# Optimization experiments

Hardware: AMD Instinct MI355X
Metric: run time of the kernel (lower is better)

Reference implementation:

```python
import jax, jax.numpy as jnp
import numpy as np

C, H, N, B, L = 1, 512, 64, 16, 2048  # n_channels, n_heads, d_kernel, batch, seq_len


def setup_inputs() -> dict:
    key = jax.random.key(0)
    k1, k2 = jax.random.split(key)
    u = jax.random.normal(k1, (B, C * H, L), dtype=jnp.float32)
    k = jax.random.normal(k2, (C, H, N), dtype=jnp.float32)
    return {"u": u, "k": k}


def _l1_normalize(x, axis):
    # torch.linalg.norm(x, ord=1, dim=axis, keepdim=True): vector 1-norm along `axis`
    return x / jnp.sum(jnp.abs(x), axis=axis, keepdims=True)


def _forward(u, k):
    c, h, n = k.shape
    bsz, d, l = u.shape  # d == c*h
    dt = u.dtype
    # Shift matrix A: A[:, :, 1:, :-1] = I  (companion-style shift)
    A = jnp.zeros((c, h, n, n), dtype=dt).at[:, :, 1:, :-1].set(jnp.eye(n - 1, dtype=dt))
    # b = e1 broadcast to (c, h, n)
    b_vec = jnp.zeros((c, h, n), dtype=dt).at[:, :, 0].set(1.0)
    # closed-loop: k_norm = L1-normalize(clamp(k, 1/16, 1)); A_cl = L1-normalize(A + b k^T)
    k_norm = _l1_normalize(jnp.clip(k, 1.0 / 16.0, 1.0), axis=2)
    BK = jnp.einsum('chi,chj->chij', b_vec, k_norm)
    M = _l1_normalize(A + BK, axis=2)

    # Krylov recurrence: f[i] = k . (M^i b), i = 0..l-1
    def step(x, _):
        f_i = jnp.einsum('chn,chn->ch', k, x)
        x_next = jnp.einsum('chij,chj->chi', M, x)
        return x_next, f_i

    _, f = jax.lax.scan(step, b_vec, None, length=l)  # f: (l, c, h)
    f = jnp.moveaxis(f, 0, -1)  # (c, h, l)

    # Causal FFT convolution of u (b, c, h, l) with filter f (c, h, l)
    n_fft = 2 * l
    uf = jnp.fft.rfft(u.reshape(bsz, c, h, l), n=n_fft)
    ff = jnp.fft.rfft(f, n=n_fft)
    y = jnp.fft.irfft(uf * ff[None], n=n_fft)[..., :l]
    return y.reshape(bsz, c * h, l)


def reference(u, k):
    return _forward(u, k)
```

## Files before the change

### kernel.cpp

```cpp
#include <hip/hip_runtime.h>


namespace {

constexpr int kH = 512;
constexpr int kL = 2048;
constexpr int kChunks = 32;
constexpr int kStride = 68;

typedef __attribute__((ext_vector_type(8))) short bf16x8;
typedef __attribute__((ext_vector_type(4))) float f32x4;

__device__ inline unsigned short f32_to_bf16_rne(float x) {
  unsigned int u = __float_as_uint(x);
  unsigned int r = u + 0x7FFFu + ((u >> 16) & 1u);
  return (unsigned short)(r >> 16);
}
__device__ inline float bf16_as_f32(unsigned short h) {
  return __uint_as_float(((unsigned int)h) << 16);
}
__device__ inline void cvt_split8(const f32x4 a, const f32x4 b, bf16x8& fh, bf16x8& fl) {
  #pragma unroll
  for (int j = 0; j < 4; ++j) {
    unsigned short hi = f32_to_bf16_rne(a[j]);
    fh[j] = (short)hi;
    fl[j] = (short)f32_to_bf16_rne(a[j] - bf16_as_f32(hi));
  }
  #pragma unroll
  for (int j = 0; j < 4; ++j) {
    unsigned short hi = f32_to_bf16_rne(b[j]);
    fh[4 + j] = (short)hi;
    fl[4 + j] = (short)f32_to_bf16_rne(b[j] - bf16_as_f32(hi));
  }
}

#define MFMA(A, B, C) __builtin_amdgcn_mfma_f32_16x16x32_bf16((A), (B), (C), 0, 0, 0)

__global__ __launch_bounds__(256, 2)
void ssm_mfma_kernel(const float* __restrict__ u,
                     const float* __restrict__ kin,
                     float* __restrict__ y) {
  const int h    = blockIdx.x;
  const int tid  = threadIdx.x;
  const int wq   = tid >> 6;
  const int lane = tid & 63;
  const int ln16 = lane & 15;
  const int quad = lane >> 4;

  __shared__ float taps[4][128];
  __shared__ float Ebuf[16][kStride];
  __shared__ float Rbuf[16][kStride];
  __shared__ float tmpA[64], cArr[64], wArr[64], gArr[64], sArr[64];

  float kv = 0.f, kc = 0.f, kn = 0.f, cc = 0.f;
  if (tid < 64) {
    kv = kin[h * 64 + tid];
    kc = fminf(fmaxf(kv, 0.0625f), 1.0f);
    tmpA[tid] = kc;
  }
  __syncthreads();
  if (tid < 64) {
    float ks = 0.f;
    for (int j = 0; j < 64; ++j) ks += tmpA[j];
    kn = kc / ks;
    cc = 1.0f / (1.0f + kn);
    cArr[tid] = cc;
  }
  __syncthreads();
  if (tid < 64) {
    float P = 1.0f;
    for (int j = 0; j < tid; ++j) P *= cArr[j];
    wArr[tid] = (tid < 63) ? (kn * cc * P) : P;
    gArr[tid] = kv * P;
    if (tid == 0) sArr[0] = 1.0f;
  }
  __syncthreads();
  float acc_s = (tid == 0) ? 1.0f : 0.0f;
  for (int rr = 0; rr < 63; ++rr) {
    if (tid < 64) {
      const float sval = sArr[rr];
      const float coef = (tid > rr) ? wArr[tid - 1 - rr] : 0.0f;
      acc_s = fmaf(coef, sval, acc_s);
      if (tid == rr + 1) sArr[tid] = acc_s;
    }
    __syncthreads();
  }
  if (tid < 128) {
    const int n = tid;
    taps[0][n] = (n < 64) ? wArr[n] : 0.0f;
    taps[1][n] = (n >= 63) ? sArr[n - 63] : 0.0f;
    taps[2][n] = (n >= 63) ? gArr[n - 63] : 0.0f;
    taps[3][n] = (n < 63) ? gArr[n + 1] : 0.0f;
  }
  __syncthreads();

  bf16x8 fragH[4][2], fragL[4][2];
  #pragma unroll
  for (int mi = 0; mi < 4; ++mi) {
    #pragma unroll
    for (int tk = 0; tk < 2; ++tk) {
      const int n0 = 16 * wq + ln16 - (32 * tk + 8 * quad) + 63;
      bf16x8 fh, fl;
      #pragma unroll
      for (int j = 0; j < 8; ++j) {
        const int n = n0 - j;
        const float v = (n >= 0 && n < 127) ? taps[mi][n] : 0.0f;
        const unsigned short hi = f32_to_bf16_rne(v);
        fh[j] = (short)hi;
        fl[j] = (short)f32_to_bf16_rne(v - bf16_as_f32(hi));
      }
      fragH[mi][tk] = fh;
      fragL[mi][tk] = fl;
    }
  }

  bf16x8 pH[2], pL[2];
  {
    bf16x8 z;
    #pragma unroll
    for (int j = 0; j < 8; ++j) z[j] = 0;
    pH[0] = z; pH[1] = z; pL[0] = z; pL[1] = z;
  }

  const size_t gbase = ((size_t)ln16 * kH + h) * kL + 16 * wq + 4 * quad;
  const float* uptr = u + gbase;
  float* yptr = y + gbase;
  const int ewrow = 16 * wq + 4 * quad;

  f32x4 unext = *(const f32x4*)(uptr);

  for (int m = 0; m < kChunks; ++m) {
    const int t0 = m * 64;
    const f32x4 ucur = unext;
    if (m + 1 < kChunks) unext = *(const f32x4*)(uptr + (m + 1) * 64);

    f32x4 accY = {};
    #pragma unroll
    for (int tk = 0; tk < 2; ++tk) {
      accY = MFMA(fragH[3][tk], pH[tk], accY);
      accY = MFMA(fragH[3][tk], pL[tk], accY);
      accY = MFMA(fragL[3][tk], pH[tk], accY);
    }
    f32x4 accE = ucur;
    #pragma unroll
    for (int tk = 0; tk < 2; ++tk) {
      accE = MFMA(fragH[0][tk], pH[tk], accE);
      accE = MFMA(fragH[0][tk], pL[tk], accE);
      accE = MFMA(fragL[0][tk], pH[tk], accE);
    }
    *(f32x4*)&Ebuf[ln16][ewrow] = accE;
    __syncthreads();

    bf16x8 eH[2], eL[2];
    #pragma unroll
    for (int tk = 0; tk < 2; ++tk) {
      const int k0 = 8 * quad + 32 * tk;
      const f32x4 a = *(const f32x4*)&Ebuf[ln16][k0];
      const f32x4 b = *(const f32x4*)&Ebuf[ln16][k0 + 4];
      cvt_split8(a, b, eH[tk], eL[tk]);
    }
    f32x4 accR = {};
    #pragma unroll
    for (int tk = 0; tk < 2; ++tk) {
      accR = MFMA(fragH[1][tk], eH[tk], accR);
      accR = MFMA(fragH[1][tk], eL[tk], accR);
      accR = MFMA(fragL[1][tk], eH[tk], accR);
    }
    *(f32x4*)&Rbuf[ln16][ewrow] = accR;
    __syncthreads();

    #pragma unroll
    for (int tk = 0; tk < 2; ++tk) {
      const int k0 = 8 * quad + 32 * tk;
      const f32x4 a = *(const f32x4*)&Rbuf[ln16][k0];
      const f32x4 b = *(const f32x4*)&Rbuf[ln16][k0 + 4];
      cvt_split8(a, b, pH[tk], pL[tk]);
    }
    #pragma unroll
    for (int tk = 0; tk < 2; ++tk) {
      accY = MFMA(fragH[2][tk], pH[tk], accY);
      accY = MFMA(fragH[2][tk], pL[tk], accY);
      accY = MFMA(fragL[2][tk], pH[tk], accY);
    }
    *(f32x4*)(yptr + t0) = accY;
  }
}

}

extern "C" void kernel_launch(void* const* d_in, const int* in_sizes, int n_in,
                              void* d_out, int out_size, void* d_ws, size_t ws_size,
                              hipStream_t stream) {
  const float* u  = (const float*)d_in[0];
  const float* kk = (const float*)d_in[1];
  if (n_in >= 2 && in_sizes[0] < in_sizes[1]) {
    const float* t = u; u = kk; kk = t;
  }
  float* y = (float*)d_out;
  hipLaunchKernelGGL(ssm_mfma_kernel, dim3(kH), dim3(256), 0, stream, u, kk, y);
}
```

Measured before the change: 146.1 us.

## Fold chunk recurrence into precomputed T matrix, single barrier per chunk

After: 155.8 us. 6.6% more time.

```diff
diff --git a/kernel.cpp b/kernel.cpp
--- a/kernel.cpp
+++ b/kernel.cpp
@@ -6,32 +6,52 @@
 constexpr int kH = 512;
 constexpr int kL = 2048;
 constexpr int kChunks = 32;
-constexpr int kStride = 68;
+constexpr int kTS = 68;
+constexpr int kPS = 68;
 
 typedef __attribute__((ext_vector_type(8))) short bf16x8;
 typedef __attribute__((ext_vector_type(4))) float f32x4;
-
-__device__ inline unsigned short f32_to_bf16_rne(float x) {
+typedef __attribute__((ext_vector_type(4))) unsigned int u32x4;
+
+__device__ inline unsigned short bf16_rne(float x) {
   unsigned int u = __float_as_uint(x);
   unsigned int r = u + 0x7FFFu + ((u >> 16) & 1u);
   return (unsigned short)(r >> 16);
 }
-__device__ inline float bf16_as_f32(unsigned short h) {
+__device__ inline float bf16f(unsigned short h) {
   return __uint_as_float(((unsigned int)h) << 16);
 }
-__device__ inline void cvt_split8(const f32x4 a, const f32x4 b, bf16x8& fh, bf16x8& fl) {
-  #pragma unroll
-  for (int j = 0; j < 4; ++j) {
-    unsigned short hi = f32_to_bf16_rne(a[j]);
-    fh[j] = (short)hi;
-    fl[j] = (short)f32_to_bf16_rne(a[j] - bf16_as_f32(hi));
-  }
-  #pragma unroll
-  for (int j = 0; j < 4; ++j) {
-    unsigned short hi = f32_to_bf16_rne(b[j]);
-    fh[4 + j] = (short)hi;
-    fl[4 + j] = (short)f32_to_bf16_rne(b[j] - bf16_as_f32(hi));
-  }
+__device__ inline unsigned pack_hi16(unsigned a, unsigned b) {
+#if __has_builtin(__builtin_amdgcn_perm)
+  return __builtin_amdgcn_perm(b, a, 0x07060302u);
+#else
+  return (b & 0xFFFF0000u) | (a >> 16);
+#endif
+}
+__device__ inline void dekker8(const f32x4 a, const f32x4 b, bf16x8& hh, bf16x8& ll) {
+  const unsigned ua0 = __float_as_uint(a[0]), ua1 = __float_as_uint(a[1]);
+  const unsigned ua2 = __float_as_uint(a[2]), ua3 = __float_as_uint(a[3]);
+  const unsigned ub0 = __float_as_uint(b[0]), ub1 = __float_as_uint(b[1]);
+  const unsigned ub2 = __float_as_uint(b[2]), ub3 = __float_as_uint(b[3]);
+  u32x4 hu, lu;
+  hu[0] = pack_hi16(ua0, ua1);
+  hu[1] = pack_hi16(ua2, ua3);
+  hu[2] = pack_hi16(ub0, ub1);
+  hu[3] = pack_hi16(ub2, ub3);
+  const float l0 = a[0] - __uint_as_float(ua0 & 0xFFFF0000u);
+  const float l1 = a[1] - __uint_as_float(ua1 & 0xFFFF0000u);
+  const float l2 = a[2] - __uint_as_float(ua2 & 0xFFFF0000u);
+  const float l3 = a[3] - __uint_as_float(ua3 & 0xFFFF0000u);
+  const float l4 = b[0] - __uint_as_float(ub0 & 0xFFFF0000u);
+  const float l5 = b[1] - __uint_as_float(ub1 & 0xFFFF0000u);
+  const float l6 = b[2] - __uint_as_float(ub2 & 0xFFFF0000u);
+  const float l7 = b[3] - __uint_as_float(ub3 & 0xFFFF0000u);
+  lu[0] = pack_hi16(__float_as_uint(l0), __float_as_uint(l1));
+  lu[1] = pack_hi16(__float_as_uint(l2), __float_as_uint(l3));
+  lu[2] = pack_hi16(__float_as_uint(l4), __float_as_uint(l5));
+  lu[3] = pack_hi16(__float_as_uint(l6), __float_as_uint(l7));
+  hh = __builtin_bit_cast(bf16x8, hu);
+  ll = __builtin_bit_cast(bf16x8, lu);
 }
 
 #define MFMA(A, B, C) __builtin_amdgcn_mfma_f32_16x16x32_bf16((A), (B), (C), 0, 0, 0)
@@ -47,10 +67,9 @@
   const int ln16 = lane & 15;
   const int quad = lane >> 4;
 
-  __shared__ float taps[4][128];
-  __shared__ float Ebuf[16][kStride];
-  __shared__ float Rbuf[16][kStride];
-  __shared__ float tmpA[64], cArr[64], wArr[64], gArr[64], sArr[64];
+  __shared__ __align__(16) float Tbuf[64][kTS];
+  __shared__ __align__(16) float Pbuf[2][16][kPS];
+  __shared__ float wArr[64], sArr[64], gArr[64], tmpA[64], cArr[64];
 
   float kv = 0.f, kc = 0.f, kn = 0.f, cc = 0.f;
   if (tid < 64) {
@@ -85,104 +104,145 @@
     }
     __syncthreads();
   }
-  if (tid < 128) {
-    const int n = tid;
-    taps[0][n] = (n < 64) ? wArr[n] : 0.0f;
-    taps[1][n] = (n >= 63) ? sArr[n - 63] : 0.0f;
-    taps[2][n] = (n >= 63) ? gArr[n - 63] : 0.0f;
-    taps[3][n] = (n < 63) ? gArr[n + 1] : 0.0f;
-  }
-  __syncthreads();
-
-  bf16x8 fragH[4][2], fragL[4][2];
+
+  const int rA = 16 * wq + ln16;
+  bf16x8 SH[2], SL[2], G1H[2], G2H[2];
   #pragma unroll
-  for (int mi = 0; mi < 4; ++mi) {
-    #pragma unroll
-    for (int tk = 0; tk < 2; ++tk) {
-      const int n0 = 16 * wq + ln16 - (32 * tk + 8 * quad) + 63;
-      bf16x8 fh, fl;
+  for (int tk = 0; tk < 2; ++tk) {
+    bf16x8 sh, sl, g1, g2;
+    #pragma unroll
+    for (int j = 0; j < 8; ++j) {
+      const int k = 32 * tk + 8 * quad + j;
+      const int d = rA - k;
+      const float sv = (d >= 0 && d < 64) ? sArr[d] : 0.0f;
+      const unsigned short shh = bf16_rne(sv);
+      sh[j] = (short)shh;
+      sl[j] = (short)bf16_rne(sv - bf16f(shh));
+      g2[j] = (short)bf16_rne((d >= 0 && d < 64) ? gArr[d] : 0.0f);
+      const int d1 = d + 64;
+      g1[j] = (short)bf16_rne((d1 >= 0 && d1 < 64) ? gArr[d1] : 0.0f);
+    }
+    SH[tk] = sh; SL[tk] = sl; G1H[tk] = g1; G2H[tk] = g2;
+  }
+
+  {
+    f32x4 accT[4];
+    #pragma unroll
+    for (int nt = 0; nt < 4; ++nt) {
+      const int col = 16 * nt + ln16;
+      f32x4 t = {};
       #pragma unroll
-      for (int j = 0; j < 8; ++j) {
-        const int n = n0 - j;
-        const float v = (n >= 0 && n < 127) ? taps[mi][n] : 0.0f;
-        const unsigned short hi = f32_to_bf16_rne(v);
-        fh[j] = (short)hi;
-        fl[j] = (short)f32_to_bf16_rne(v - bf16_as_f32(hi));
+      for (int tk = 0; tk < 2; ++tk) {
+        bf16x8 wh, wl;
+        #pragma unroll
+        for (int j = 0; j < 8; ++j) {
+          const int k = 32 * tk + 8 * quad + j;
+          const int idx = 63 + k - col;
+          const float wv = (idx >= 0 && idx < 64) ? wArr[idx] : 0.0f;
+          const unsigned short whh = bf16_rne(wv);
+          wh[j] = (short)whh;
+          wl[j] = (short)bf16_rne(wv - bf16f(whh));
+        }
+        t = MFMA(SH[tk], wh, t);
+        t = MFMA(SH[tk], wl, t);
+        t = MFMA(SL[tk], wh, t);
       }
-      fragH[mi][tk] = fh;
-      fragL[mi][tk] = fl;
-    }
-  }
-
-  bf16x8 pH[2], pL[2];
+      accT[nt] = t;
+    }
+    #pragma unroll
+    for (int nt = 0; nt < 4; ++nt)
+      #pragma unroll
+      for (int reg = 0; reg < 4; ++reg)
+        Tbuf[16 * wq + 4 * quad + reg][16 * nt + ln16] = accT[nt][reg];
+  }
+  __syncthreads();
+
+  bf16x8 TH[2], TL[2];
+  #pragma unroll
+  for (int tk = 0; tk < 2; ++tk) {
+    const f32x4 ta = *(const f32x4*)&Tbuf[rA][32 * tk + 8 * quad];
+    const f32x4 tb = *(const f32x4*)&Tbuf[rA][32 * tk + 8 * quad + 4];
+    bf16x8 th, tl;
+    #pragma unroll
+    for (int j = 0; j < 4; ++j) {
+      unsigned short x = bf16_rne(ta[j]);
+      th[j] = (short)x; tl[j] = (short)bf16_rne(ta[j] - bf16f(x));
+      unsigned short z = bf16_rne(tb[j]);
+      th[4 + j] = (short)z; tl[4 + j] = (short)bf16_rne(tb[j] - bf16f(z));
+    }
+    TH[tk] = th; TL[tk] = tl;
+  }
+
+  const size_t bstr = (size_t)kH * kL;
+  const float* ub = u + (size_t)ln16 * bstr + (size_t)h * kL;
+  float* yb = y + (size_t)ln16 * bstr + (size_t)h * kL + 16 * wq + 4 * quad;
+
+  bf16x8 uHf[2], uLf[2], pH[2], pL[2];
   {
     bf16x8 z;
     #pragma unroll
     for (int j = 0; j < 8; ++j) z[j] = 0;
     pH[0] = z; pH[1] = z; pL[0] = z; pL[1] = z;
   }
-
-  const size_t gbase = ((size_t)ln16 * kH + h) * kL + 16 * wq + 4 * quad;
-  const float* uptr = u + gbase;
-  float* yptr = y + gbase;
-  const int ewrow = 16 * wq + 4 * quad;
-
-  f32x4 unext = *(const f32x4*)(uptr);
+  #pragma unroll
+  for (int tk = 0; tk < 2; ++tk) {
+    const f32x4 a = *(const f32x4*)(ub + 32 * tk + 8 * quad);
+    const f32x4 b = *(const f32x4*)(ub + 32 * tk + 8 * quad + 4);
+    dekker8(a, b, uHf[tk], uLf[tk]);
+  }
 
   for (int m = 0; m < kChunks; ++m) {
     const int t0 = m * 64;
-    const f32x4 ucur = unext;
-    if (m + 1 < kChunks) unext = *(const f32x4*)(uptr + (m + 1) * 64);
+    f32x4 na0, nb0, na1, nb1;
+    if (m + 1 < kChunks) {
+      const float* up = ub + t0 + 64 + 8 * quad;
+      na0 = *(const f32x4*)(up);
+      nb0 = *(const f32x4*)(up + 4);
+      na1 = *(const f32x4*)(up + 32);
+      nb1 = *(const f32x4*)(up + 32 + 4);
+    }
+
+    f32x4 accSu = {};
+    #pragma unroll
+    for (int tk = 0; tk < 2; ++tk) {
+      accSu = MFMA(SH[tk], uHf[tk], accSu);
+      accSu = MFMA(SH[tk], uLf[tk], accSu);
+      accSu = MFMA(SL[tk], uHf[tk], accSu);
+    }
+    f32x4 accTp = {};
+    #pragma unroll
+    for (int tk = 0; tk < 2; ++tk) {
+      accTp = MFMA(TH[tk], pH[tk], accTp);
+      accTp = MFMA(TH[tk], pL[tk], accTp);
+      accTp = MFMA(TL[tk], pH[tk], accTp);
+    }
+    const f32x4 accP = accSu + accTp;
+    *(f32x4*)&Pbuf[m & 1][ln16][16 * wq + 4 * quad] = accP;
 
     f32x4 accY = {};
     #pragma unroll
     for (int tk = 0; tk < 2; ++tk) {
-      accY = MFMA(fragH[3][tk], pH[tk], accY);
-      accY = MFMA(fragH[3][tk], pL[tk], accY);
-      accY = MFMA(fragL[3][tk], pH[tk], accY);
-    }
-    f32x4 accE = ucur;
-    #pragma unroll
-    for (int tk = 0; tk < 2; ++tk) {
-      accE = MFMA(fragH[0][tk], pH[tk], accE);
-      accE = MFMA(fragH[0][tk], pL[tk], accE);
-      accE = MFMA(fragL[0][tk], pH[tk], accE);
-    }
-    *(f32x4*)&Ebuf[ln16][ewrow] = accE;
+      accY = MFMA(G1H[tk], pH[tk], accY);
+      accY = MFMA(G1H[tk], pL[tk], accY);
+    }
+    if (m + 1 < kChunks) {
+      dekker8(na0, nb0, uHf[0], uLf[0]);
+      dekker8(na1, nb1, uHf[1], uLf[1]);
+    }
     __syncthreads();
 
-    bf16x8 eH[2], eL[2];
-    #pragma unroll
-    for (int tk = 0; tk < 2; ++tk) {
-      const int k0 = 8 * quad + 32 * tk;
-      const f32x4 a = *(const f32x4*)&Ebuf[ln16][k0];
-      const f32x4 b = *(const f32x4*)&Ebuf[ln16][k0 + 4];
-      cvt_split8(a, b, eH[tk], eL[tk]);
-    }
-    f32x4 accR = {};
-    #pragma unroll
-    for (int tk = 0; tk < 2; ++tk) {
-      accR = MFMA(fragH[1][tk], eH[tk], accR);
-      accR = MFMA(fragH[1][tk], eL[tk], accR);
-      accR = MFMA(fragL[1][tk], eH[tk], accR);
-    }
-    *(f32x4*)&Rbuf[ln16][ewrow] = accR;
-    __syncthreads();
-
-    #pragma unroll
-    for (int tk = 0; tk < 2; ++tk) {
-      const int k0 = 8 * quad + 32 * tk;
-      const f32x4 a = *(const f32x4*)&Rbuf[ln16][k0];
-      const f32x4 b = *(const f32x4*)&Rbuf[ln16][k0 + 4];
-      cvt_split8(a, b, pH[tk], pL[tk]);
-    }
-    #pragma unroll
-    for (int tk = 0; tk < 2; ++tk) {
-      accY = MFMA(fragH[2][tk], pH[tk], accY);
-      accY = MFMA(fragH[2][tk], pL[tk], accY);
-      accY = MFMA(fragL[2][tk], pH[tk], accY);
-    }
-    *(f32x4*)(yptr + t0) = accY;
+    #pragma unroll
+    for (int tk = 0; tk < 2; ++tk) {
+      const f32x4 pa = *(const f32x4*)&Pbuf[m & 1][ln16][32 * tk + 8 * quad];
+      const f32x4 pb = *(const f32x4*)&Pbuf[m & 1][ln16][32 * tk + 8 * quad + 4];
+      dekker8(pa, pb, pH[tk], pL[tk]);
+    }
+    #pragma unroll
+    for (int tk = 0; tk < 2; ++tk) {
+      accY = MFMA(G2H[tk], pH[tk], accY);
+      accY = MFMA(G2H[tk], pL[tk], accY);
+    }
+    *(f32x4*)(yb + t0) = accY;
   }
 }
 
```
